# Kernel tuning notes

Measured on AMD Instinct MI355X. Metric: run time of the kernel, lower is better.

Reference implementation:

```python
import jax, jax.numpy as jnp
import numpy as np

HEADS = 8
DIM_HEAD = 64
NB_FEATURES = 256
CHUNK = 128          # chunk size used by performer's causal_linear_attention_noncuda
EPS_KERNEL = 1e-4    # eps in softmax_kernel feature map
EPS_DENOM = 1e-6     # eps added to k_cumsum in the denominator


def softmax_kernel(data, proj, is_query):
    # FAVOR+ positive softmax random features (performer_pytorch.softmax_kernel)
    # data: [B,H,N,D], proj: [M,D]
    d = data.shape[-1]
    normalizer = d ** -0.25
    ratio = proj.shape[0] ** -0.5
    data_dash = jnp.einsum('bhnd,md->bhnm', data * normalizer, proj)
    # ||x||^2 / (2*sqrt(d))
    diag = jnp.sum(data * data, axis=-1, keepdims=True) * 0.5 * (normalizer ** 2)
    if is_query:
        m = jax.lax.stop_gradient(jnp.max(data_dash, axis=-1, keepdims=True))
    else:
        m = jax.lax.stop_gradient(jnp.max(data_dash, axis=(-1, -2), keepdims=True))
    return ratio * (jnp.exp(data_dash - diag - m) + EPS_KERNEL)


def causal_linear_attention(qp, kp, v, chunk=CHUNK):
    # Chunked causal linear attention (O(N) in seq len):
    # out_i = q'_i . S_i / (q'_i . z_i), S_i = sum_{j<=i} k'_j v_j^T, z_i = cumsum k'_j
    B, H, N, M = qp.shape
    E = v.shape[-1]
    C = N // chunk

    def to_chunks(x):
        return x.reshape(B, H, C, chunk, x.shape[-1]).transpose(2, 0, 1, 3, 4)

    qc, kc, vc = to_chunks(qp), to_chunks(kp), to_chunks(v)
    k0 = jnp.zeros((B, H, M), qp.dtype)
    s0 = jnp.zeros((B, H, M, E), qp.dtype)

    def step(carry, inp):
        k_last, s_last = carry
        q, k, vv = inp  # [B,H,c,M], [B,H,c,M], [B,H,c,E]
        k_cum = k_last[:, :, None, :] + jnp.cumsum(k, axis=2)           # [B,H,c,M]
        d_inv = 1.0 / jnp.einsum('bhnm,bhnm->bhn', q, k_cum + EPS_DENOM)
        ctx = jnp.einsum('bhnm,bhne->bhnme', k, vv)                      # [B,H,c,M,E]
        s_cum = s_last[:, :, None] + jnp.cumsum(ctx, axis=2)             # [B,H,c,M,E]
        out = jnp.einsum('bhnme,bhnm,bhn->bhne', s_cum, q, d_inv)        # [B,H,c,E]
        return (k_cum[:, :, -1, :], s_cum[:, :, -1]), out

    _, outs = jax.lax.scan(step, (k0, s0), (qc, kc, vc))  # [C,B,H,c,E]
    return outs.transpose(1, 2, 0, 3, 4).reshape(B, H, N, E)


def setup_inputs() -> dict:
    key = jax.random.key(0)
    k1, k2, k3, k4 = jax.random.split(key, 4)
    B, N, D = 4, 2048, 512
    return {
        'query': jax.random.normal(k1, (B, N, D), jnp.float32),
        'key': jax.random.normal(k2, (B, N, D), jnp.float32),
        'value': jax.random.normal(k3, (B, N, D), jnp.float32),
        'projection': jax.random.normal(k4, (NB_FEATURES, DIM_HEAD), jnp.float32),
    }


def reference(query, key, value, projection):
    B, N, D = query.shape

    def split(x):  # [B,N,D] -> [B,H,N,Dh]
        return x.reshape(B, N, HEADS, DIM_HEAD).transpose(0, 2, 1, 3)

    q, k, v = split(query), split(key), split(value)
    qp = softmax_kernel(q, projection, is_query=True)
    kp = softmax_kernel(k, projection, is_query=False)
    out = causal_linear_attention(qp, kp, v)
    return out.transpose(0, 2, 1, 3).reshape(B, N, D)
```

## Files before the change

kernel.cpp:

```cpp
#include <hip/hip_runtime.h>
#include <math.h>

#define BB 4
#define NN 2048
#define DD 512
#define HH 8
#define DH 64
#define MM 256
#define BH 32
#define CHK 128
#define NCH 16
#define ROWS (BH*NN)

constexpr float NRM   = 0.35355339059327373f;
constexpr float RATIO = 0.0625f;
constexpr float EPSK  = 1e-4f;
constexpr float EPSD  = 1e-6f;

#define OFFB_QP   ((size_t)0)
#define OFFB_SP   ((size_t)33554432)
#define OFFB_KP   (OFFB_SP + (size_t)16777216)
#define OFFB_VT   (OFFB_KP + (size_t)33554432)
#define OFFB_Z    (OFFB_VT + (size_t)8388608)
#define OFFB_KMP  (OFFB_Z  + (size_t)524288)
#define OFFB_PJB  (OFFB_KMP + (size_t)4096)

typedef __attribute__((ext_vector_type(8))) short short8;
typedef __attribute__((ext_vector_type(4))) float f32x4;

__device__ __forceinline__ float b2f(ushort u) {
  union { float f; unsigned int i; } x; x.i = ((unsigned int)u) << 16; return x.f;
}
__device__ __forceinline__ ushort f2b(float f) {
  unsigned int u = __float_as_uint(f);
  unsigned int r = (u + 0x7FFFu + ((u >> 16) & 1u)) >> 16;
  return (ushort)r;
}

#define MFMA(a,b,c) __builtin_amdgcn_mfma_f32_16x16x32_bf16(a, b, c, 0, 0, 0)

__global__ __launch_bounds__(256) void prep_kernel(const float* __restrict__ proj,
                                                   char* __restrict__ ws) {
  const int i = blockIdx.x*256 + threadIdx.x;
  float4 v = *(const float4*)(proj + (size_t)i*4);
  ushort4 o;
  o.x = f2b(v.x); o.y = f2b(v.y); o.z = f2b(v.z); o.w = f2b(v.w);
  *(ushort4*)((ushort*)(ws + OFFB_PJB) + (size_t)i*4) = o;
}

template<int MODE>
__device__ __forceinline__ void featm_body(const float* __restrict__ inp,
                                           const ushort* __restrict__ projb,
                                           char* __restrict__ ws,
                                           char* lds, int blk) {
  ushort* xh = (ushort*)lds;
  ushort* xl = xh + 64*72;
  ushort* ps = xl + 64*72;
  ushort* qt = (ushort*)lds;
  float* diag_s = (float*)(lds + 36864);
  float (*wmax)[4] = (float(*)[4])(lds + 37120);
  float* kred = (float*)(lds + 38144);

  const int t  = threadIdx.x;
  const int w  = t >> 6;
  const int l  = t & 63;
  const int lq = l >> 4;
  const int ln = l & 15;

  const int rowbase = blk * 64;
  const int bh = rowbase >> 11;
  const int b  = bh >> 3, h = bh & 7;
  const int n0 = rowbase & (NN - 1);

  {
    const int r  = t >> 2;
    const int c0 = (t & 3) * 16;
    const float* src = inp + ((size_t)(b*NN + n0 + r))*DD + h*DH + c0;
    float vv[16];
    #pragma unroll
    for (int j = 0; j < 4; ++j) {
      float4 v = *(const float4*)(src + j*4);
      vv[4*j+0] = v.x*NRM; vv[4*j+1] = v.y*NRM;
      vv[4*j+2] = v.z*NRM; vv[4*j+3] = v.w*NRM;
    }
    float s = 0.f;
    ushort hi[16], lo[16];
    #pragma unroll
    for (int j = 0; j < 16; ++j) {
      s += vv[j]*vv[j];
      hi[j] = f2b(vv[j]);
      lo[j] = f2b(vv[j] - b2f(hi[j]));
    }
    *(short8*)(xh + r*72 + c0)     = *(short8*)&hi[0];
    *(short8*)(xh + r*72 + c0 + 8) = *(short8*)&hi[8];
    *(short8*)(xl + r*72 + c0)     = *(short8*)&lo[0];
    *(short8*)(xl + r*72 + c0 + 8) = *(short8*)&lo[8];
    s += __shfl_xor(s, 1); s += __shfl_xor(s, 2);
    if ((t & 3) == 0) diag_s[r] = 0.5f * s;
  }

  f32x4 acc[4][4];
  #pragma unroll
  for (int mt = 0; mt < 4; ++mt)
    #pragma unroll
    for (int c = 0; c < 4; ++c) acc[mt][c] = (f32x4){0.f,0.f,0.f,0.f};

  #pragma unroll
  for (int p = 0; p < 2; ++p) {
    if (p) __syncthreads();
    #pragma unroll
    for (int ld = 0; ld < 4; ++ld) {
      int flat = t + 256*ld;
      int r = flat >> 3, g = flat & 7;
      *(short8*)(ps + r*72 + g*8) = *(const short8*)(projb + (size_t)(p*128 + r)*DH + g*8);
    }
    __syncthreads();
    #pragma unroll
    for (int kk = 0; kk < 2; ++kk) {
      short8 ah[4], al[4];
      #pragma unroll
      for (int mt = 0; mt < 4; ++mt) {
        ah[mt] = *(const short8*)(xh + (mt*16 + ln)*72 + kk*32 + lq*8);
        al[mt] = *(const short8*)(xl + (mt*16 + ln)*72 + kk*32 + lq*8);
      }
      #pragma unroll
      for (int ntl = 0; ntl < 2; ++ntl) {
        short8 bf = *(const short8*)(ps + (w*32 + ntl*16 + ln)*72 + kk*32 + lq*8);
        #pragma unroll
        for (int mt = 0; mt < 4; ++mt) {
          acc[mt][2*p+ntl] = MFMA(al[mt], bf, acc[mt][2*p+ntl]);
          acc[mt][2*p+ntl] = MFMA(ah[mt], bf, acc[mt][2*p+ntl]);
        }
      }
    }
  }

  if (MODE == 1) {
    float mx = -1e30f;
    #pragma unroll
    for (int mt = 0; mt < 4; ++mt)
      #pragma unroll
      for (int c = 0; c < 4; ++c)
        #pragma unroll
        for (int reg = 0; reg < 4; ++reg) mx = fmaxf(mx, acc[mt][c][reg]);
    #pragma unroll
    for (int m = 1; m < 64; m <<= 1) mx = fmaxf(mx, __shfl_xor(mx, m));
    if (l == 0) kred[w] = mx;
    __syncthreads();
    if (t == 0)
      ((float*)(ws + OFFB_KMP))[blk] =
        fmaxf(fmaxf(kred[0], kred[1]), fmaxf(kred[2], kred[3]));
    return;
  }

  if (MODE == 0) {
    #pragma unroll
    for (int mt = 0; mt < 4; ++mt)
      #pragma unroll
      for (int reg = 0; reg < 4; ++reg) {
        float m = acc[mt][0][reg];
        #pragma unroll
        for (int c = 1; c < 4; ++c) m = fmaxf(m, acc[mt][c][reg]);
        m = fmaxf(m, __shfl_xor(m, 1));
        m = fmaxf(m, __shfl_xor(m, 2));
        m = fmaxf(m, __shfl_xor(m, 4));
        m = fmaxf(m, __shfl_xor(m, 8));
        if (ln == 0) wmax[mt*16 + lq*4 + reg][w] = m;
      }
  }
  if (MODE == 2) {
    if (t < 32) {
      float m = ((const float*)(ws + OFFB_KMP))[bh*32 + t];
      #pragma unroll
      for (int d = 1; d < 32; d <<= 1) m = fmaxf(m, __shfl_xor(m, d));
      if (t == 0) kred[0] = m;
    }
  }
  __syncthreads();

  float km = 0.f;
  if (MODE == 2) km = kred[0];

  #pragma unroll
  for (int mt = 0; mt < 4; ++mt)
    #pragma unroll
    for (int reg = 0; reg < 4; ++reg) {
      const int row = mt*16 + lq*4 + reg;
      float rm;
      if (MODE == 0) {
        float4 wm4 = *(const float4*)&wmax[row][0];
        rm = fmaxf(fmaxf(wm4.x, wm4.y), fmaxf(wm4.z, wm4.w));
      } else {
        rm = km;
      }
      const float dg = diag_s[row];
      #pragma unroll
      for (int c = 0; c < 4; ++c) {
        const int f = (c >> 1)*128 + w*32 + (c & 1)*16 + ln;
        qt[row*264 + f] = f2b(RATIO*(__expf(acc[mt][c][reg] - dg - rm) + EPSK));
      }
    }
  __syncthreads();

  ushort* dstbase = (ushort*)(ws + (MODE == 0 ? OFFB_QP : OFFB_KP)) + (size_t)rowbase*MM;
  #pragma unroll
  for (int ld = 0; ld < 8; ++ld) {
    int flat = t + 256*ld;
    int row = flat >> 5, g = flat & 31;
    *(short8*)(dstbase + (size_t)row*MM + g*8) = *(const short8*)(qt + row*264 + g*8);
  }
}

__device__ __forceinline__ void vt_body(const float* __restrict__ value,
                                        char* __restrict__ ws,
                                        char* lds, int blk) {
  float (*vsh)[68] = (float(*)[68])lds;
  const int t = threadIdx.x;
  const int bh = blk >> 4, nc = blk & 15;
  const int b = bh >> 3, h = bh & 7;
  const int n0 = nc * CHK;
  #pragma unroll
  for (int l = 0; l < 8; ++l) {
    int flat = t + 256*l;
    int r = flat >> 4, g = flat & 15;
    *(float4*)&vsh[r][g*4] = *(const float4*)(value + ((size_t)(b*NN + n0 + r))*DD + h*DH + g*4);
  }
  __syncthreads();
  const int e = t & 63, qd = t >> 6;
  ushort* vt = (ushort*)(ws + OFFB_VT) + ((size_t)bh*DH + e)*NN + n0 + qd*32;
  #pragma unroll
  for (int p = 0; p < 16; ++p) {
    unsigned int lo = f2b(vsh[qd*32 + 2*p][e]);
    unsigned int hi = f2b(vsh[qd*32 + 2*p + 1][e]);
    ((unsigned int*)vt)[p] = lo | (hi << 16);
  }
}

__global__ __launch_bounds__(256) void mega_kernel(const float* __restrict__ q,
                                                   const float* __restrict__ k,
                                                   const float* __restrict__ v,
                                                   char* __restrict__ ws) {
  __shared__ __align__(16) char lds[38160];
  const ushort* projb = (const ushort*)(ws + OFFB_PJB);
  const int blk = blockIdx.x;
  if (blk < 1024)       featm_body<0>(q, projb, ws, lds, blk);
  else if (blk < 2048)  featm_body<1>(k, projb, ws, lds, blk - 1024);
  else                  vt_body(v, ws, lds, blk - 2048);
}

__global__ __launch_bounds__(256) void featm2_kernel(const float* __restrict__ k,
                                                     char* __restrict__ ws) {
  __shared__ __align__(16) char lds[38160];
  featm_body<2>(k, (const ushort*)(ws + OFFB_PJB), ws, lds, blockIdx.x);
}

__global__ __launch_bounds__(256) void sprefix_kernel(char* __restrict__ ws) {
  __shared__ __align__(16) unsigned int kpTu[16*68];
  __shared__ __align__(16) ushort Vts[64*136];
  __shared__ float zred[16][16];

  const int t  = threadIdx.x;
  const int w  = t >> 6;
  const int l  = t & 63;
  const int lq = l >> 4;
  const int ln = l & 15;
  const int bh = blockIdx.x >> 4;
  const int ms = blockIdx.x & 15;

  const ushort* kpb = (const ushort*)(ws + OFFB_KP) + (size_t)bh*NN*MM + ms*16;
  const ushort* vtb = (const ushort*)(ws + OFFB_VT) + (size_t)bh*DH*NN;
  ushort* spb = (ushort*)(ws + OFFB_SP) + (size_t)bh*NCH*DH*MM + ms*16;
  float*  zb  = (float*)(ws + OFFB_Z) + (size_t)bh*NCH*MM + ms*16;

  f32x4 acc = (f32x4){0.f,0.f,0.f,0.f};
  float zrun = 0.f;

  for (int tc = 0; tc < NCH; ++tc) {
    __syncthreads();

    if (t < 16) {
      if (tc > 0) {
        float s = 0.f;
        #pragma unroll
        for (int q = 0; q < 16; ++q) s += zred[q][t];
        zrun += s;
      }
      zb[(size_t)tc*MM + t] = zrun;
    }
    {
      ushort* sp = spb + (size_t)tc*DH*MM;
      #pragma unroll
      for (int reg = 0; reg < 4; ++reg)
        sp[(size_t)(w*16 + lq*4 + reg)*MM + ln] = f2b(acc[reg]);
    }

    const ushort* kslice = kpb + (size_t)tc*CHK*MM;
    if (t < 128) {
      int jp = t >> 1, mo = t & 1;
      short8 a = *(const short8*)(kslice + (size_t)(2*jp)*MM + mo*8);
      short8 c = *(const short8*)(kslice + (size_t)(2*jp+1)*MM + mo*8);
      #pragma unroll
      for (int i = 0; i < 8; ++i) {
        unsigned int u = (unsigned int)(unsigned short)a[i]
                       | ((unsigned int)(unsigned short)c[i] << 16);
        kpTu[(mo*8 + i)*68 + jp] = u;
      }
    }
    #pragma unroll
    for (int it = 0; it < 4; ++it) {
      int slot = t + 256*it;
      int e = slot >> 4, g = slot & 15;
      *(short8*)(Vts + e*136 + g*8) = *(const short8*)(vtb + (size_t)e*NN + tc*CHK + g*8);
    }
    __syncthreads();

    {
      int m = t & 15, q = t >> 4;
      float s = 0.f;
      #pragma unroll
      for (int u = 0; u < 4; ++u) {
        unsigned int p = kpTu[m*68 + q*4 + u];
        s += b2f((ushort)(p & 0xFFFF)) + b2f((ushort)(p >> 16));
      }
      zred[q][m] = s;
    }

    #pragma unroll
    for (int kk = 0; kk < 4; ++kk) {
      short8 af = *(const short8*)(Vts + (w*16 + ln)*136 + kk*32 + lq*8);
      short8 bf = *(const short8*)((const ushort*)kpTu + (size_t)ln*136 + kk*32 + lq*8);
      acc = MFMA(af, bf, acc);
    }
  }
}

__global__ __launch_bounds__(256) void fused_kernel(float* __restrict__ out,
                                                    char* __restrict__ ws) {
  __shared__ __align__(16) char lds[52224];
  __shared__ float den_i[128];
  __shared__ float dinv_s[128];

  const int t  = threadIdx.x;
  const int w  = t >> 6;
  const int l  = t & 63;
  const int lq = l >> 4;
  const int ln = l & 15;
  const int rt0 = w;
  const int rt1 = 7 - w;
  const int blk = blockIdx.x;
  const int bh = blk >> 4, tc = blk & 15;
  const int b = bh >> 3, h = bh & 7;
  const size_t rowbase = (size_t)bh*NN + tc*CHK;

  const ushort* qpg = (const ushort*)(ws + OFFB_QP) + rowbase*MM;
  const ushort* kpg = (const ushort*)(ws + OFFB_KP) + rowbase*MM;

  ushort* qs = (ushort*)lds;
  ushort* ks = qs + 128*72;

  f32x4 acc[2][8];
  #pragma unroll
  for (int mt = 0; mt < 2; ++mt)
    #pragma unroll
    for (int nt = 0; nt < 8; ++nt) acc[mt][nt] = (f32x4){0.f,0.f,0.f,0.f};

  for (int mc = 0; mc < 4; ++mc) {
    __syncthreads();
    #pragma unroll
    for (int ld2 = 0; ld2 < 4; ++ld2) {
      int flat = t + 256*ld2; int r = flat >> 3, g = flat & 7;
      *(short8*)(qs + r*72 + g*8) = *(const short8*)(qpg + (size_t)r*MM + mc*64 + g*8);
      *(short8*)(ks + r*72 + g*8) = *(const short8*)(kpg + (size_t)r*MM + mc*64 + g*8);
    }
    __syncthreads();
    #pragma unroll
    for (int kk = 0; kk < 2; ++kk) {
      short8 af0 = *(const short8*)(qs + (rt0*16 + ln)*72 + kk*32 + lq*8);
      short8 af1 = *(const short8*)(qs + (rt1*16 + ln)*72 + kk*32 + lq*8);
      #pragma unroll
      for (int nt = 0; nt < 8; ++nt) {
        if (nt <= rt1) {
          short8 bf = *(const short8*)(ks + (nt*16 + ln)*72 + kk*32 + lq*8);
          if (nt <= rt0) acc[0][nt] = MFMA(af0, bf, acc[0][nt]);
          acc[1][nt] = MFMA(af1, bf, acc[1][nt]);
        }
      }
    }
  }

  __syncthreads();

  ushort* P   = (ushort*)lds;
  ushort* Vts = (ushort*)(lds + 34816);

  float rs[2][4] = {{0,0,0,0},{0,0,0,0}};
  #pragma unroll
  for (int mt = 0; mt < 2; ++mt) {
    const int ibase = (mt ? rt1 : rt0) * 16;
    #pragma unroll
    for (int nt = 0; nt < 8; ++nt)
      #pragma unroll
      for (int reg = 0; reg < 4; ++reg) {
        int i = ibase + lq*4 + reg;
        int j = nt*16 + ln;
        float v = (j <= i) ? acc[mt][nt][reg] : 0.f;
        rs[mt][reg] += v;
        P[i*136 + j] = f2b(v);
      }
  }
  #pragma unroll
  for (int mt = 0; mt < 2; ++mt) {
    const int ibase = (mt ? rt1 : rt0) * 16;
    #pragma unroll
    for (int reg = 0; reg < 4; ++reg) {
      float s = rs[mt][reg];
      s += __shfl_xor(s, 1); s += __shfl_xor(s, 2);
      s += __shfl_xor(s, 4); s += __shfl_xor(s, 8);
      if (ln == 0) den_i[ibase + lq*4 + reg] = s;
    }
  }

  const ushort* vtg = (const ushort*)(ws + OFFB_VT) + (size_t)bh*DH*NN + tc*CHK;
  #pragma unroll
  for (int ld2 = 0; ld2 < 4; ++ld2) {
    int flat = t + 256*ld2; int e = flat >> 4, g = flat & 15;
    *(short8*)(Vts + e*136 + g*8) = *(const short8*)(vtg + (size_t)e*NN + g*8);
  }
  __syncthreads();

  {
    const float* zp = (const float*)(ws + OFFB_Z) + (size_t)blk*MM;
    const int r = t >> 1, hf = t & 1;
    const ushort* qrow = qpg + (size_t)r*MM + hf*128;
    float s = 0.f;
    #pragma unroll
    for (int g = 0; g < 16; ++g) {
      short8 qv = *(const short8*)(qrow + g*8);
      const float* zz = zp + hf*128 + g*8;
      #pragma unroll
      for (int x = 0; x < 8; ++x)
        s += b2f((ushort)qv[x]) * (zz[x] + EPSD);
    }
    s += __shfl_xor(s, 1);
    if (hf == 0) dinv_s[r] = 1.0f / (s + den_i[r]);
  }

  f32x4 oacc[2][4];
  #pragma unroll
  for (int mt = 0; mt < 2; ++mt)
    #pragma unroll
    for (int nt = 0; nt < 4; ++nt) oacc[mt][nt] = (f32x4){0.f,0.f,0.f,0.f};

  #pragma unroll
  for (int kk = 0; kk < 4; ++kk) {
    short8 af0 = *(const short8*)(P + (rt0*16 + ln)*136 + kk*32 + lq*8);
    short8 af1 = *(const short8*)(P + (rt1*16 + ln)*136 + kk*32 + lq*8);
    #pragma unroll
    for (int nt = 0; nt < 4; ++nt) {
      short8 bf = *(const short8*)(Vts + (nt*16 + ln)*136 + kk*32 + lq*8);
      oacc[0][nt] = MFMA(af0, bf, oacc[0][nt]);
      oacc[1][nt] = MFMA(af1, bf, oacc[1][nt]);
    }
  }
  __syncthreads();

  ushort* qs2 = (ushort*)lds;
  ushort* ss  = qs2 + 128*72;
  const ushort* spg = (const ushort*)(ws + OFFB_SP) + (size_t)blk*DH*MM;
  for (int mc = 0; mc < 4; ++mc) {
    if (mc) __syncthreads();
    #pragma unroll
    for (int ld2 = 0; ld2 < 4; ++ld2) {
      int flat = t + 256*ld2; int r = flat >> 3, g = flat & 7;
      *(short8*)(qs2 + r*72 + g*8) = *(const short8*)(qpg + (size_t)r*MM + mc*64 + g*8);
    }
    #pragma unroll
    for (int ld2 = 0; ld2 < 2; ++ld2) {
      int flat = t + 256*ld2; int e = flat >> 3, g = flat & 7;
      *(short8*)(ss + e*72 + g*8) = *(const short8*)(spg + (size_t)e*MM + mc*64 + g*8);
    }
    __syncthreads();
    #pragma unroll
    for (int kk = 0; kk < 2; ++kk) {
      short8 af0 = *(const short8*)(qs2 + (rt0*16 + ln)*72 + kk*32 + lq*8);
      short8 af1 = *(const short8*)(qs2 + (rt1*16 + ln)*72 + kk*32 + lq*8);
      #pragma unroll
      for (int nt = 0; nt < 4; ++nt) {
        short8 bf = *(const short8*)(ss + (nt*16 + ln)*72 + kk*32 + lq*8);
        oacc[0][nt] = MFMA(af0, bf, oacc[0][nt]);
        oacc[1][nt] = MFMA(af1, bf, oacc[1][nt]);
      }
    }
  }

  #pragma unroll
  for (int mt = 0; mt < 2; ++mt) {
    const int ibase = (mt ? rt1 : rt0) * 16;
    #pragma unroll
    for (int reg = 0; reg < 4; ++reg) {
      const int i = ibase + lq*4 + reg;
      const float di = dinv_s[i];
      float* dst = out + ((size_t)(b*NN) + tc*CHK + i)*DD + h*DH;
      #pragma unroll
      for (int nt = 0; nt < 4; ++nt)
        dst[nt*16 + ln] = oacc[mt][nt][reg] * di;
    }
  }
}

extern "C" void kernel_launch(void* const* d_in, const int* in_sizes, int n_in,
                              void* d_out, int out_size, void* d_ws, size_t ws_size,
                              hipStream_t stream) {
  (void)in_sizes; (void)n_in; (void)out_size; (void)ws_size;
  const float* q    = (const float*)d_in[0];
  const float* k    = (const float*)d_in[1];
  const float* v    = (const float*)d_in[2];
  const float* proj = (const float*)d_in[3];
  float* out = (float*)d_out;
  char*  ws  = (char*)d_ws;

  prep_kernel<<<16, 256, 0, stream>>>(proj, ws);
  mega_kernel<<<2560, 256, 0, stream>>>(q, k, v, ws);
  featm2_kernel<<<1024, 256, 0, stream>>>(k, ws);
  sprefix_kernel<<<512, 256, 0, stream>>>(ws);
  fused_kernel<<<512, 256, 0, stream>>>(out, ws);
}
```

Baseline: 191.0 us.

## Replace second key feature pass with per-block max rescaling factors

Instead of recomputing the key projection a second time once the global per-head max is known, the first pass stores exp(x - diag - blockmax) and a tiny kernel computes per-block scale factors RATIO*exp(blockmax - globalmax). These factors are applied, together with the eps term, when the key features are loaded in the prefix and fused kernels. The fused kernel also merges the q·S inter-chunk matmul into the first q·k loop, so q tiles are loaded only once. The cost is extra bf16 rescale arithmetic at load time and an added rounding step, which could slightly change accuracy.

Measured after the change: 187.9 us. No clear change (-1.6%).

```diff
diff --git a/kernel.cpp b/kernel.cpp
--- a/kernel.cpp
+++ b/kernel.cpp
@@ -16,6 +16,7 @@
 constexpr float RATIO = 0.0625f;
 constexpr float EPSK  = 1e-4f;
 constexpr float EPSD  = 1e-6f;
+constexpr float REPS  = 0.0625f * 1e-4f;
 
 #define OFFB_QP   ((size_t)0)
 #define OFFB_SP   ((size_t)33554432)
@@ -23,7 +24,8 @@
 #define OFFB_VT   (OFFB_KP + (size_t)33554432)
 #define OFFB_Z    (OFFB_VT + (size_t)8388608)
 #define OFFB_KMP  (OFFB_Z  + (size_t)524288)
-#define OFFB_PJB  (OFFB_KMP + (size_t)4096)
+#define OFFB_SF   (OFFB_KMP + (size_t)4096)
+#define OFFB_PJB  (OFFB_SF + (size_t)4096)
 
 typedef __attribute__((ext_vector_type(8))) short short8;
 typedef __attribute__((ext_vector_type(4))) float f32x4;
@@ -135,24 +137,6 @@
     }
   }
 
-  if (MODE == 1) {
-    float mx = -1e30f;
-    #pragma unroll
-    for (int mt = 0; mt < 4; ++mt)
-      #pragma unroll
-      for (int c = 0; c < 4; ++c)
-        #pragma unroll
-        for (int reg = 0; reg < 4; ++reg) mx = fmaxf(mx, acc[mt][c][reg]);
-    #pragma unroll
-    for (int m = 1; m < 64; m <<= 1) mx = fmaxf(mx, __shfl_xor(mx, m));
-    if (l == 0) kred[w] = mx;
-    __syncthreads();
-    if (t == 0)
-      ((float*)(ws + OFFB_KMP))[blk] =
-        fmaxf(fmaxf(kred[0], kred[1]), fmaxf(kred[2], kred[3]));
-    return;
-  }
-
   if (MODE == 0) {
     #pragma unroll
     for (int mt = 0; mt < 4; ++mt)
@@ -167,19 +151,25 @@
         m = fmaxf(m, __shfl_xor(m, 8));
         if (ln == 0) wmax[mt*16 + lq*4 + reg][w] = m;
       }
-  }
-  if (MODE == 2) {
-    if (t < 32) {
-      float m = ((const float*)(ws + OFFB_KMP))[bh*32 + t];
-      #pragma unroll
-      for (int d = 1; d < 32; d <<= 1) m = fmaxf(m, __shfl_xor(m, d));
-      if (t == 0) kred[0] = m;
-    }
+  } else {
+    float mx = -1e30f;
+    #pragma unroll
+    for (int mt = 0; mt < 4; ++mt)
+      #pragma unroll
+      for (int c = 0; c < 4; ++c)
+        #pragma unroll
+        for (int reg = 0; reg < 4; ++reg) mx = fmaxf(mx, acc[mt][c][reg]);
+    #pragma unroll
+    for (int m = 1; m < 64; m <<= 1) mx = fmaxf(mx, __shfl_xor(mx, m));
+    if (l == 0) kred[w] = mx;
   }
   __syncthreads();
 
   float km = 0.f;
-  if (MODE == 2) km = kred[0];
+  if (MODE == 1) {
+    km = fmaxf(fmaxf(kred[0], kred[1]), fmaxf(kred[2], kred[3]));
+    if (t == 0) ((float*)(ws + OFFB_KMP))[blk] = km;
+  }
 
   #pragma unroll
   for (int mt = 0; mt < 4; ++mt)
@@ -197,7 +187,8 @@
       #pragma unroll
       for (int c = 0; c < 4; ++c) {
         const int f = (c >> 1)*128 + w*32 + (c & 1)*16 + ln;
-        qt[row*264 + f] = f2b(RATIO*(__expf(acc[mt][c][reg] - dg - rm) + EPSK));
+        const float e = __expf(acc[mt][c][reg] - dg - rm);
+        qt[row*264 + f] = f2b(MODE == 0 ? RATIO*(e + EPSK) : e);
       }
     }
   __syncthreads();
@@ -248,10 +239,14 @@
   else                  vt_body(v, ws, lds, blk - 2048);
 }
 
-__global__ __launch_bounds__(256) void featm2_kernel(const float* __restrict__ k,
-                                                     char* __restrict__ ws) {
-  __shared__ __align__(16) char lds[38160];
-  featm_body<2>(k, (const ushort*)(ws + OFFB_PJB), ws, lds, blockIdx.x);
+__global__ __launch_bounds__(256) void sfac_kernel(char* __restrict__ ws) {
+  const int blk = blockIdx.x*256 + threadIdx.x;
+  const int bh = blk >> 5;
+  const float* kmp = (const float*)(ws + OFFB_KMP);
+  float km = -1e30f;
+  #pragma unroll
+  for (int i = 0; i < 32; ++i) km = fmaxf(km, kmp[bh*32 + i]);
+  ((float*)(ws + OFFB_SF))[blk] = RATIO * __expf(kmp[blk] - km);
 }
 
 __global__ __launch_bounds__(256) void sprefix_kernel(char* __restrict__ ws) {
@@ -269,6 +264,7 @@
 
   const ushort* kpb = (const ushort*)(ws + OFFB_KP) + (size_t)bh*NN*MM + ms*16;
   const ushort* vtb = (const ushort*)(ws + OFFB_VT) + (size_t)bh*DH*NN;
+  const float*  sf  = (const float*)(ws + OFFB_SF);
   ushort* spb = (ushort*)(ws + OFFB_SP) + (size_t)bh*NCH*DH*MM + ms*16;
   float*  zb  = (float*)(ws + OFFB_Z) + (size_t)bh*NCH*MM + ms*16;
 
@@ -297,13 +293,14 @@
     const ushort* kslice = kpb + (size_t)tc*CHK*MM;
     if (t < 128) {
       int jp = t >> 1, mo = t & 1;
+      float s0 = sf[bh*32 + tc*2 + (jp >> 5)];
       short8 a = *(const short8*)(kslice + (size_t)(2*jp)*MM + mo*8);
       short8 c = *(const short8*)(kslice + (size_t)(2*jp+1)*MM + mo*8);
       #pragma unroll
       for (int i = 0; i < 8; ++i) {
-        unsigned int u = (unsigned int)(unsigned short)a[i]
-                       | ((unsigned int)(unsigned short)c[i] << 16);
-        kpTu[(mo*8 + i)*68 + jp] = u;
+        ushort ua = f2b(fmaf(b2f((ushort)a[i]), s0, REPS));
+        ushort uc = f2b(fmaf(b2f((ushort)c[i]), s0, REPS));
+        kpTu[(mo*8 + i)*68 + jp] = (unsigned int)ua | ((unsigned int)uc << 16);
       }
     }
     #pragma unroll
@@ -354,15 +351,24 @@
 
   const ushort* qpg = (const ushort*)(ws + OFFB_QP) + rowbase*MM;
   const ushort* kpg = (const ushort*)(ws + OFFB_KP) + rowbase*MM;
+  const ushort* spg = (const ushort*)(ws + OFFB_SP) + (size_t)blk*DH*MM;
+  const float*  sf  = (const float*)(ws + OFFB_SF);
+  const float sc0 = sf[blk*2], sc1 = sf[blk*2 + 1];
 
   ushort* qs = (ushort*)lds;
   ushort* ks = qs + 128*72;
+  ushort* ss = ks + 128*72;
 
   f32x4 acc[2][8];
   #pragma unroll
   for (int mt = 0; mt < 2; ++mt)
     #pragma unroll
     for (int nt = 0; nt < 8; ++nt) acc[mt][nt] = (f32x4){0.f,0.f,0.f,0.f};
+  f32x4 oacc[2][4];
+  #pragma unroll
+  for (int mt = 0; mt < 2; ++mt)
+    #pragma unroll
+    for (int nt = 0; nt < 4; ++nt) oacc[mt][nt] = (f32x4){0.f,0.f,0.f,0.f};
 
   for (int mc = 0; mc < 4; ++mc) {
     __syncthreads();
@@ -370,7 +376,21 @@
     for (int ld2 = 0; ld2 < 4; ++ld2) {
       int flat = t + 256*ld2; int r = flat >> 3, g = flat & 7;
       *(short8*)(qs + r*72 + g*8) = *(const short8*)(qpg + (size_t)r*MM + mc*64 + g*8);
-      *(short8*)(ks + r*72 + g*8) = *(const short8*)(kpg + (size_t)r*MM + mc*64 + g*8);
+    }
+    #pragma unroll
+    for (int ld2 = 0; ld2 < 4; ++ld2) {
+      int flat = t + 256*ld2; int r = flat >> 3, g = flat & 7;
+      short8 kv = *(const short8*)(kpg + (size_t)r*MM + mc*64 + g*8);
+      const float sc = (r & 64) ? sc1 : sc0;
+      ushort ov[8];
+      #pragma unroll
+      for (int i = 0; i < 8; ++i) ov[i] = f2b(fmaf(b2f((ushort)kv[i]), sc, REPS));
+      *(short8*)(ks + r*72 + g*8) = *(short8*)&ov[0];
+    }
+    #pragma unroll
+    for (int ld2 = 0; ld2 < 2; ++ld2) {
+      int flat = t + 256*ld2; int e = flat >> 3, g = flat & 7;
+      *(short8*)(ss + e*72 + g*8) = *(const short8*)(spg + (size_t)e*MM + mc*64 + g*8);
     }
     __syncthreads();
     #pragma unroll
@@ -385,6 +405,12 @@
           acc[1][nt] = MFMA(af1, bf, acc[1][nt]);
         }
       }
+      #pragma unroll
+      for (int nt = 0; nt < 4; ++nt) {
+        short8 bf = *(const short8*)(ss + (nt*16 + ln)*72 + kk*32 + lq*8);
+        oacc[0][nt] = MFMA(af0, bf, oacc[0][nt]);
+        oacc[1][nt] = MFMA(af1, bf, oacc[1][nt]);
+      }
     }
   }
 
@@ -444,12 +470,7 @@
     s += __shfl_xor(s, 1);
     if (hf == 0) dinv_s[r] = 1.0f / (s + den_i[r]);
   }
-
-  f32x4 oacc[2][4];
-  #pragma unroll
-  for (int mt = 0; mt < 2; ++mt)
-    #pragma unroll
-    for (int nt = 0; nt < 4; ++nt) oacc[mt][nt] = (f32x4){0.f,0.f,0.f,0.f};
+  __syncthreads();
 
   #pragma unroll
   for (int kk = 0; kk < 4; ++kk) {
@@ -460,36 +481,6 @@
       short8 bf = *(const short8*)(Vts + (nt*16 + ln)*136 + kk*32 + lq*8);
       oacc[0][nt] = MFMA(af0, bf, oacc[0][nt]);
       oacc[1][nt] = MFMA(af1, bf, oacc[1][nt]);
-    }
-  }
-  __syncthreads();
-
-  ushort* qs2 = (ushort*)lds;
-  ushort* ss  = qs2 + 128*72;
-  const ushort* spg = (const ushort*)(ws + OFFB_SP) + (size_t)blk*DH*MM;
-  for (int mc = 0; mc < 4; ++mc) {
-    if (mc) __syncthreads();
-    #pragma unroll
-    for (int ld2 = 0; ld2 < 4; ++ld2) {
-      int flat = t + 256*ld2; int r = flat >> 3, g = flat & 7;
-      *(short8*)(qs2 + r*72 + g*8) = *(const short8*)(qpg + (size_t)r*MM + mc*64 + g*8);
-    }
-    #pragma unroll
-    for (int ld2 = 0; ld2 < 2; ++ld2) {
-      int flat = t + 256*ld2; int e = flat >> 3, g = flat & 7;
-      *(short8*)(ss + e*72 + g*8) = *(const short8*)(spg + (size_t)e*MM + mc*64 + g*8);
-    }
-    __syncthreads();
-    #pragma unroll
-    for (int kk = 0; kk < 2; ++kk) {
-      short8 af0 = *(const short8*)(qs2 + (rt0*16 + ln)*72 + kk*32 + lq*8);
-      short8 af1 = *(const short8*)(qs2 + (rt1*16 + ln)*72 + kk*32 + lq*8);
-      #pragma unroll
-      for (int nt = 0; nt < 4; ++nt) {
-        short8 bf = *(const short8*)(ss + (nt*16 + ln)*72 + kk*32 + lq*8);
-        oacc[0][nt] = MFMA(af0, bf, oacc[0][nt]);
-        oacc[1][nt] = MFMA(af1, bf, oacc[1][nt]);
-      }
     }
   }
 
@@ -521,7 +512,7 @@
 
   prep_kernel<<<16, 256, 0, stream>>>(proj, ws);
   mega_kernel<<<2560, 256, 0, stream>>>(q, k, v, ws);
-  featm2_kernel<<<1024, 256, 0, stream>>>(k, ws);
+  sfac_kernel<<<4, 256, 0, stream>>>(ws);
   sprefix_kernel<<<512, 256, 0, stream>>>(ws);
   fused_kernel<<<512, 256, 0, stream>>>(out, ws);
 }
```
